# Kernel optimization log

Hardware: AMD Instinct MI355X
Metric: run time of the kernel (lower is better)

## Reference

```python
import jax, jax.numpy as jnp
import numpy as np

EPS = 1e-8
ALPHA = 0.3
PATTERN_W = 0.1


def setup_inputs() -> dict:
    key = jax.random.key(0)
    ks = jax.random.split(key, 6)
    H, W, D, Hid = 1024, 1024, 32, 64
    return {
        "grid_states": jax.random.normal(ks[0], (H, W, D), dtype=jnp.float32),
        "potentials": jax.random.uniform(ks[1], (H, W), dtype=jnp.float32),
        "W1": jax.random.normal(ks[2], (D + 1, Hid), dtype=jnp.float32) * 0.1,
        "b1": jax.random.normal(ks[3], (Hid,), dtype=jnp.float32) * 0.1,
        "W2": jax.random.normal(ks[4], (Hid, D), dtype=jnp.float32) * 0.1,
        "b2": jax.random.normal(ks[5], (D,), dtype=jnp.float32) * 0.1,
    }


def reference(grid_states, potentials, W1, b1, W2, b2):
    # self_similarity: A^3 normalized to unit length, rescaled by ||A||
    cube = grid_states * grid_states * grid_states                     # [H,W,D]
    cube_norm = jnp.linalg.norm(cube, axis=-1, keepdims=True)          # [H,W,1]
    cell_norm = jnp.linalg.norm(grid_states, axis=-1, keepdims=True)   # [H,W,1]
    self_pattern = cube / (cube_norm + EPS) * cell_norm                # [H,W,D]

    cell_with_pattern = grid_states + PATTERN_W * self_pattern         # [H,W,D]

    # transform_net on [cell_with_pattern ; potential]
    x = jnp.concatenate([cell_with_pattern, potentials[..., None]], axis=-1)  # [H,W,D+1]
    h = jax.nn.relu(jnp.einsum("hwc,cf->hwf", x, W1) + b1)             # [H,W,Hid]
    transformed = jnp.einsum("hwf,fd->hwd", h, W2) + b2                # [H,W,D]

    # new_state = transform + alpha * cell  (neighbor influence path only
    # affects role_value, which forward() discards)
    return transformed + ALPHA * grid_states
```

## Files before the change

kernel.cpp:

```cpp
#include <hip/hip_runtime.h>

#define DIM   32
#define HID   64
#define TILES 8

typedef __attribute__((ext_vector_type(8))) short bf16x8;
typedef __attribute__((ext_vector_type(4))) float f32x4;

__device__ __forceinline__ unsigned cvt_pk_bf16(float lo, float hi) {
    unsigned r;
    asm("v_cvt_pk_bf16_f32 %0, %1, %2" : "=v"(r) : "v"(lo), "v"(hi));
    return r;
}

__device__ __forceinline__ void plswap(unsigned &a, unsigned &b) {
    auto r = __builtin_amdgcn_permlane32_swap((int)a, (int)b, false, false);
    a = (unsigned)r[0];
    b = (unsigned)r[1];
}

__device__ __forceinline__ float quad_sum(float x) {
    unsigned a = __float_as_uint(x), b = __float_as_uint(x);
    plswap(a, b);
    float t = __uint_as_float(a) + __uint_as_float(b);
    return t + __shfl_xor(t, 16, 64);
}

union bfu { bf16x8 v; unsigned u[4]; };

__global__ __launch_bounds__(256, 4) void behavior_mfma(
    const float* __restrict__ g_in,
    const float* __restrict__ pot,
    const float* __restrict__ W1,
    const float* __restrict__ b1,
    const float* __restrict__ W2,
    const float* __restrict__ b2,
    float* __restrict__ out)
{
    const int tid  = threadIdx.x;
    const int lane = tid & 63;
    const int quad = lane >> 4;
    const int mrow = lane & 15;
    const int wave = tid >> 6;

    bf16x8 w1f[4];
    #pragma unroll
    for (int nb = 0; nb < 4; ++nb) {
        bfu t;
        #pragma unroll
        for (int jp = 0; jp < 4; ++jp)
            t.u[jp] = cvt_pk_bf16(W1[(quad * 8 + 2 * jp)     * HID + nb * 16 + mrow],
                                  W1[(quad * 8 + 2 * jp + 1) * HID + nb * 16 + mrow]);
        w1f[nb] = t.v;
    }
    bf16x8 w2f[2][2];
    #pragma unroll
    for (int kc = 0; kc < 2; ++kc)
        #pragma unroll
        for (int nc = 0; nc < 2; ++nc) {
            bfu t;
            #pragma unroll
            for (int jp = 0; jp < 4; ++jp) {
                const int j0 = 2 * jp;
                const int r0 = kc * 32 + (quad >> 1) * 16 + (quad & 1) * 4
                             + ((j0 >> 2) << 3) + (j0 & 3);
                t.u[jp] = cvt_pk_bf16(W2[r0 * DIM + nc * 16 + mrow],
                                      W2[(r0 + 1) * DIM + nc * 16 + mrow]);
            }
            w2f[kc][nc] = t.v;
        }
    bf16x8 aid[2];
    #pragma unroll
    for (int nc = 0; nc < 2; ++nc) {
        bfu t;
        #pragma unroll
        for (int jp = 0; jp < 4; ++jp) {
            unsigned lo = (quad * 8 + 2 * jp     == nc * 16 + mrow) ? 0x00003F80u : 0u;
            unsigned hi = (quad * 8 + 2 * jp + 1 == nc * 16 + mrow) ? 0x3F800000u : 0u;
            t.u[jp] = lo | hi;
        }
        aid[nc] = t.v;
    }
    float w1pq[4][4], b1q[4][4];
    #pragma unroll
    for (int nb = 0; nb < 4; ++nb)
        #pragma unroll
        for (int r = 0; r < 4; ++r) {
            w1pq[nb][r] = W1[32 * HID + nb * 16 + quad * 4 + r];
            b1q[nb][r]  = b1[nb * 16 + quad * 4 + r];
        }
    float b2q[2][4];
    #pragma unroll
    for (int nc = 0; nc < 2; ++nc)
        #pragma unroll
        for (int r = 0; r < 4; ++r)
            b2q[nc][r] = b2[nc * 16 + quad * 4 + r];

    const long cell0 = ((long)blockIdx.x * 4 + wave) * (TILES * 16);

    float4 gA[2], gB[2]; float pV[2];
    auto loadT = [&](long cb, int s) {
        const float* gp = g_in + (cb + mrow) * DIM + quad * 8;
        gA[s] = ((const float4*)gp)[0];
        gB[s] = ((const float4*)gp)[1];
        pV[s] = pot[cb + mrow];
    };
    loadT(cell0, 0);
    loadT(cell0 + 16, 1);

    #pragma unroll 2
    for (int t = 0; t < TILES; ++t) {
        const int s = t & 1;
        const long cb = cell0 + (long)t * 16;
        const float4 a = gA[s], b = gB[s];
        const float potv = pV[s];

        float gv[8] = {a.x, a.y, a.z, a.w, b.x, b.y, b.z, b.w};
        float cube[8];
        float tp = 0.f, sp = 0.f;
        #pragma unroll
        for (int j = 0; j < 8; ++j) {
            float gc = gv[j];
            float g2 = gc * gc;
            float g3 = g2 * gc;
            tp += g2;
            sp = fmaf(g3, g3, sp);
            cube[j] = g3;
        }
        tp = quad_sum(tp);
        sp = quad_sum(sp);
        const float scale = 0.1f * __builtin_amdgcn_sqrtf(tp) *
                            __builtin_amdgcn_rcpf(__builtin_amdgcn_sqrtf(sp) + 1e-8f);

        bfu xf, gf;
        #pragma unroll
        for (int jp = 0; jp < 4; ++jp) {
            xf.u[jp] = cvt_pk_bf16(fmaf(scale, cube[2 * jp],     gv[2 * jp]),
                                   fmaf(scale, cube[2 * jp + 1], gv[2 * jp + 1]));
            gf.u[jp] = cvt_pk_bf16(0.3f * gv[2 * jp], 0.3f * gv[2 * jp + 1]);
        }

        if (t + 2 < TILES) loadT(cb + 32, s);

        unsigned P[4][2];
        #pragma unroll
        for (int nb = 0; nb < 4; ++nb) {
            f32x4 c1;
            #pragma unroll
            for (int r = 0; r < 4; ++r)
                c1[r] = fmaf(potv, w1pq[nb][r], b1q[nb][r]);
            c1 = __builtin_amdgcn_mfma_f32_16x16x32_bf16(w1f[nb], xf.v, c1, 0, 0, 0);
            P[nb][0] = cvt_pk_bf16(fmaxf(c1[0], 0.f), fmaxf(c1[1], 0.f));
            P[nb][1] = cvt_pk_bf16(fmaxf(c1[2], 0.f), fmaxf(c1[3], 0.f));
        }

        bfu h0, h1;
        {
            unsigned x0 = P[0][0], y0 = P[1][0]; plswap(x0, y0);
            unsigned x1 = P[0][1], y1 = P[1][1]; plswap(x1, y1);
            h0.u[0] = x0; h0.u[1] = x1; h0.u[2] = y0; h0.u[3] = y1;
        }
        {
            unsigned x0 = P[2][0], y0 = P[3][0]; plswap(x0, y0);
            unsigned x1 = P[2][1], y1 = P[3][1]; plswap(x1, y1);
            h1.u[0] = x0; h1.u[1] = x1; h1.u[2] = y0; h1.u[3] = y1;
        }

        #pragma unroll
        for (int nc = 0; nc < 2; ++nc) {
            f32x4 c2 = {b2q[nc][0], b2q[nc][1], b2q[nc][2], b2q[nc][3]};
            c2 = __builtin_amdgcn_mfma_f32_16x16x32_bf16(aid[nc],    gf.v, c2, 0, 0, 0);
            c2 = __builtin_amdgcn_mfma_f32_16x16x32_bf16(w2f[0][nc], h0.v, c2, 0, 0, 0);
            c2 = __builtin_amdgcn_mfma_f32_16x16x32_bf16(w2f[1][nc], h1.v, c2, 0, 0, 0);
            f32x4* op = (f32x4*)(out + (cb + mrow) * DIM + nc * 16 + quad * 4);
            __builtin_nontemporal_store(c2, op);
        }
    }
}

extern "C" void kernel_launch(void* const* d_in, const int* in_sizes, int n_in,
                              void* d_out, int out_size, void* d_ws, size_t ws_size,
                              hipStream_t stream) {
    const float* g_in = (const float*)d_in[0];
    const float* pot  = (const float*)d_in[1];
    const float* W1   = (const float*)d_in[2];
    const float* b1   = (const float*)d_in[3];
    const float* W2   = (const float*)d_in[4];
    const float* b2   = (const float*)d_in[5];
    float* out = (float*)d_out;

    const int n_cells = in_sizes[1];
    const int cells_per_block = 4 * TILES * 16;
    const int blocks = (n_cells + cells_per_block - 1) / cells_per_block;

    behavior_mfma<<<blocks, 256, 0, stream>>>(g_in, pot, W1, b1, W2, b2, out);
}
```

Measured before the change: 256.2 us.

## Deepen prefetch to four tiles, hoist loads above weight setup, use permlane16 reduction

The first four tiles of grid and potential data are now loaded before the weight fragments are converted, so the initial memory latency overlaps with setup. The loop is fully unrolled and processes tiles in pairs with a four-deep register prefetch ring, and the output stores for each pair are grouped after the next loads are issued. Stores become plain instead of nontemporal, and the cross-quad reduction uses permlane16_swap instead of a shuffle. This raises register pressure, which could hurt occupancy under launch_bounds(256,4), and the plain stores may pollute the cache.

```diff
diff --git a/kernel.cpp b/kernel.cpp
--- a/kernel.cpp
+++ b/kernel.cpp
@@ -20,10 +20,12 @@
 }
 
 __device__ __forceinline__ float quad_sum(float x) {
-    unsigned a = __float_as_uint(x), b = __float_as_uint(x);
-    plswap(a, b);
-    float t = __uint_as_float(a) + __uint_as_float(b);
-    return t + __shfl_xor(t, 16, 64);
+    auto r1 = __builtin_amdgcn_permlane32_swap(__float_as_int(x), __float_as_int(x),
+                                               false, false);
+    float t = __int_as_float(r1[0]) + __int_as_float(r1[1]);
+    auto r2 = __builtin_amdgcn_permlane16_swap(__float_as_int(t), __float_as_int(t),
+                                               false, false);
+    return __int_as_float(r2[0]) + __int_as_float(r2[1]);
 }
 
 union bfu { bf16x8 v; unsigned u[4]; };
@@ -43,6 +45,18 @@
     const int mrow = lane & 15;
     const int wave = tid >> 6;
 
+    const long cell0 = ((long)blockIdx.x * 4 + wave) * (TILES * 16);
+
+    float4 gA[4], gB[4]; float pV[4];
+    auto loadT = [&](int s, long cb) {
+        const float* gp = g_in + (cb + mrow) * DIM + quad * 8;
+        gA[s] = ((const float4*)gp)[0];
+        gB[s] = ((const float4*)gp)[1];
+        pV[s] = pot[cb + mrow];
+    };
+    #pragma unroll
+    for (int s = 0; s < 4; ++s) loadT(s, cell0 + (long)s * 16);
+
     bf16x8 w1f[4];
     #pragma unroll
     for (int nb = 0; nb < 4; ++nb) {
@@ -96,22 +110,7 @@
         for (int r = 0; r < 4; ++r)
             b2q[nc][r] = b2[nc * 16 + quad * 4 + r];
 
-    const long cell0 = ((long)blockIdx.x * 4 + wave) * (TILES * 16);
-
-    float4 gA[2], gB[2]; float pV[2];
-    auto loadT = [&](long cb, int s) {
-        const float* gp = g_in + (cb + mrow) * DIM + quad * 8;
-        gA[s] = ((const float4*)gp)[0];
-        gB[s] = ((const float4*)gp)[1];
-        pV[s] = pot[cb + mrow];
-    };
-    loadT(cell0, 0);
-    loadT(cell0 + 16, 1);
-
-    #pragma unroll 2
-    for (int t = 0; t < TILES; ++t) {
-        const int s = t & 1;
-        const long cb = cell0 + (long)t * 16;
+    auto computeT = [&](int s, f32x4& o0, f32x4& o1) {
         const float4 a = gA[s], b = gB[s];
         const float potv = pV[s];
 
@@ -139,8 +138,6 @@
                                    fmaf(scale, cube[2 * jp + 1], gv[2 * jp + 1]));
             gf.u[jp] = cvt_pk_bf16(0.3f * gv[2 * jp], 0.3f * gv[2 * jp + 1]);
         }
-
-        if (t + 2 < TILES) loadT(cb + 32, s);
 
         unsigned P[4][2];
         #pragma unroll
@@ -172,9 +169,28 @@
             c2 = __builtin_amdgcn_mfma_f32_16x16x32_bf16(aid[nc],    gf.v, c2, 0, 0, 0);
             c2 = __builtin_amdgcn_mfma_f32_16x16x32_bf16(w2f[0][nc], h0.v, c2, 0, 0, 0);
             c2 = __builtin_amdgcn_mfma_f32_16x16x32_bf16(w2f[1][nc], h1.v, c2, 0, 0, 0);
-            f32x4* op = (f32x4*)(out + (cb + mrow) * DIM + nc * 16 + quad * 4);
-            __builtin_nontemporal_store(c2, op);
-        }
+            if (nc == 0) o0 = c2; else o1 = c2;
+        }
+    };
+
+    #pragma unroll
+    for (int g = 0; g < 4; ++g) {
+        const int s0 = (2 * g) & 3, s1 = (2 * g + 1) & 3;
+        f32x4 o0, o1, o2, o3;
+        computeT(s0, o0, o1);
+        computeT(s1, o2, o3);
+
+        if (g < 2) {
+            loadT(s0, cell0 + (long)(2 * g + 4) * 16);
+            loadT(s1, cell0 + (long)(2 * g + 5) * 16);
+        }
+
+        const long cb0 = cell0 + (long)(2 * g) * 16;
+        const long cb1 = cell0 + (long)(2 * g + 1) * 16;
+        *(f32x4*)(out + (cb0 + mrow) * DIM +  0 + quad * 4) = o0;
+        *(f32x4*)(out + (cb0 + mrow) * DIM + 16 + quad * 4) = o1;
+        *(f32x4*)(out + (cb1 + mrow) * DIM +  0 + quad * 4) = o2;
+        *(f32x4*)(out + (cb1 + mrow) * DIM + 16 + quad * 4) = o3;
     }
 }
 
```

Measured after the change: 325.6 us. +27.1%, slower.
